# Kernel optimization log

Hardware: AMD Instinct MI355X
Metric: run time of the kernel (lower is better)

The kernel has to match this reference:

```python
import jax, jax.numpy as jnp
import numpy as np

SEQ, DM, NH, DH = 8192, 1024, 16, 64


def setup_inputs() -> dict:
    key = jax.random.key(0)
    k = jax.random.split(key, 8)
    return {
        "xs": jax.random.normal(k[0], (SEQ, DM), dtype=jnp.float32),
        "wq": jax.random.normal(k[1], (NH, DH, DM), dtype=jnp.float32),
        "wk": jax.random.normal(k[2], (NH, DH, DM), dtype=jnp.float32),
        "wv": jax.random.normal(k[3], (NH, DH, DM), dtype=jnp.float32),
        # MLP: Linear(NH*DH -> DM), gelu, Linear(DM -> NH*DH); eqx stores W as (out, in)
        "w1": jax.random.normal(k[4], (DM, NH * DH), dtype=jnp.float32) * 0.02,
        "b1": jnp.zeros((DM,), dtype=jnp.float32),
        "w2": jax.random.normal(k[5], (NH * DH, DM), dtype=jnp.float32) * 0.02,
        "b2": jnp.zeros((NH * DH,), dtype=jnp.float32),
    }


def _act(x):
    return jax.nn.elu(x) + 1.0


def reference(xs, wq, wk, wv, w1, b1, w2, b2):
    # project: (n_heads d_head d_model),(seq d_model) -> (seq n_heads d_head)
    q = jnp.einsum('hdm,sm->shd', wq, xs)
    k = jnp.einsum('hdm,sm->shd', wk, xs)
    v = jnp.einsum('hdm,sm->shd', wv, xs)

    def cell(state, qkv):
        s, z = state                      # s: (h, dk, dv), z: (h, dk)
        qt, kt, vt = qkv                  # each (h, d)
        kt = _act(kt)
        s = s + jnp.einsum('hk,hv->hkv', kt, vt)
        z = z + kt
        qa = _act(qt)
        # faithful to einops 'n_heads d_head_k d_head_v, n_heads d_head_q -> n_heads d_head_v'
        sq = jnp.einsum('hkv,hq->hv', s, qa)
        zq = jnp.einsum('hk,hq->h', z, qa)
        return (s, z), sq / zq[:, None]

    init = (jnp.zeros((NH, DH, DH), xs.dtype), jnp.zeros((NH, DH), xs.dtype))
    _, out = jax.lax.scan(cell, init, (q, k, v))   # out: (seq, h, d)
    out = out.reshape(SEQ, NH * DH)
    h = jax.nn.gelu(out @ w1.T + b1)
    return h @ w2.T + b2
```

## Files before the change

### kernel.cpp

```cpp
#include <hip/hip_runtime.h>
#include <hip/hip_bf16.h>

using bf16 = __hip_bfloat16;
typedef __attribute__((ext_vector_type(8))) short shortx8;
typedef __attribute__((ext_vector_type(4))) float f32x4;

#define SEQ 8192
#define DM 1024
#define NH 16
#define CHUNK 64
#define NC (SEQ / CHUNK)
#define NT (DM / 64)

__device__ __forceinline__ void load_lds16(const bf16* g, bf16* l) {
    __builtin_amdgcn_global_load_lds(
        (const __attribute__((address_space(1))) void*)g,
        (__attribute__((address_space(3))) void*)l, 16, 0, 0);
}

__device__ __forceinline__ unsigned ldsoff(const bf16* p) {
    return (unsigned)(unsigned long long)(__attribute__((address_space(3))) const void*)p;
}

__device__ __forceinline__ shortx8 dsr128(unsigned a) {
    shortx8 r;
    asm volatile("ds_read_b128 %0, %1" : "=v"(r) : "v"(a));
    return r;
}

__device__ __forceinline__ float bf2f(short s) {
    union { unsigned u; float f; } x;
    x.u = ((unsigned)(unsigned short)s) << 16;
    return x.f;
}

__global__ __launch_bounds__(256) void convert_all(const float* __restrict__ xs,
                                                   const float* __restrict__ wk,
                                                   const float* __restrict__ wv,
                                                   const float* __restrict__ w1,
                                                   const float* __restrict__ w2,
                                                   bf16* __restrict__ xsb,
                                                   bf16* __restrict__ wall) {
    const int b = blockIdx.x;
    const float* in;
    bf16* out;
    int blk;
    if (b < 8192) {
        in = xs; out = xsb; blk = b;
    } else {
        const int seg = (b - 8192) >> 10;
        blk = (b - 8192) & 1023;
        out = wall + (size_t)seg * DM * DM;
        if (seg == 0)      in = wk;
        else if (seg == 1) in = wv;
        else if (seg == 2) in = w1;
        else               in = w2;
    }
    size_t i = ((size_t)blk * 256 + threadIdx.x) * 4;
    float4 f = *(const float4*)(in + i);
    out[i + 0] = __float2bfloat16(f.x);
    out[i + 1] = __float2bfloat16(f.y);
    out[i + 2] = __float2bfloat16(f.z);
    out[i + 3] = __float2bfloat16(f.w);
}

template <int MODE>
__global__ __launch_bounds__(512, 2) void gemm256(const bf16* __restrict__ A,
                                                  const bf16* __restrict__ B,
                                                  void* __restrict__ Cv,
                                                  const float* __restrict__ bias,
                                                  float* __restrict__ kappa,
                                                  int N) {
    __shared__ __align__(16) bf16 As[2][256][64];
    __shared__ __align__(16) bf16 Bs[2][256][64];

    const int tid = threadIdx.x;
    const int nwg = gridDim.x * gridDim.y;
    const int bid = blockIdx.x + blockIdx.y * gridDim.x;
    const int cpx = nwg >> 3;
    const int swz = (bid & 7) * cpx + (bid >> 3);
    const int ry  = swz % gridDim.y;
    const int rx  = swz / gridDim.y;
    const int bm  = ry * 256;
    const int bn  = rx * 256;

    const int wave = tid >> 6;
    const int lane = tid & 63;
    const int wr   = wave >> 2;
    const int wc   = wave & 3;
    const int quad = lane >> 4;
    const int m16  = lane & 15;
    const int r7   = m16 & 7;
    const int wr128 = wr * 128;
    const int wc64  = wc * 64;
    const int kp0 = ((quad ^ r7) * 8);
    const int kp1 = (((4 + quad) ^ r7) * 8);

    auto stageA = [&](int half, int kt) {
        #pragma unroll
        for (int it = 0; it < 2; ++it) {
            int s = it * 512 + tid;
            int row = s >> 3, pos = s & 7;
            int g = pos ^ (row & 7);
            load_lds16(A + (size_t)(bm + half * 128 + row) * DM + kt * 64 + g * 8,
                       &As[kt & 1][half * 128 + row][pos * 8]);
        }
    };
    auto stageB = [&](int half, int kt) {
        #pragma unroll
        for (int it = 0; it < 2; ++it) {
            int s = it * 512 + tid;
            int row = s >> 3, pos = s & 7;
            int g = pos ^ (row & 7);
            load_lds16(B + (size_t)(bn + half * 128 + row) * DM + kt * 64 + g * 8,
                       &Bs[kt & 1][half * 128 + row][pos * 8]);
        }
    };

    f32x4 acc[8][4];
    #pragma unroll
    for (int i = 0; i < 8; ++i)
        #pragma unroll
        for (int j = 0; j < 4; ++j)
            #pragma unroll
            for (int r = 0; r < 4; ++r) acc[i][j][r] = 0.f;

    stageA(0, 0); stageA(1, 0); stageB(0, 0); stageB(1, 0);
    stageB(0, 1); stageB(1, 1);
    asm volatile("s_waitcnt vmcnt(4)");
    __builtin_amdgcn_s_barrier();

    shortx8 af[4][2], blo[2][2], bhi[2][2];

    #pragma unroll 1
    for (int t = 0; t < NT; ++t) {
        const int sl = t & 1;
        if (t + 1 < NT) { stageA(0, t + 1); stageA(1, t + 1); }
        #pragma unroll
        for (int i = 0; i < 4; ++i) {
            af[i][0] = dsr128(ldsoff(&As[sl][wr128 + i * 16 + m16][kp0]));
            af[i][1] = dsr128(ldsoff(&As[sl][wr128 + i * 16 + m16][kp1]));
        }
        #pragma unroll
        for (int j = 0; j < 2; ++j) {
            blo[j][0] = dsr128(ldsoff(&Bs[sl][wc64 + j * 16 + m16][kp0]));
            blo[j][1] = dsr128(ldsoff(&Bs[sl][wc64 + j * 16 + m16][kp1]));
            bhi[j][0] = dsr128(ldsoff(&Bs[sl][wc64 + (j + 2) * 16 + m16][kp0]));
            bhi[j][1] = dsr128(ldsoff(&Bs[sl][wc64 + (j + 2) * 16 + m16][kp1]));
        }
        asm volatile("s_waitcnt lgkmcnt(0)");
        __builtin_amdgcn_sched_barrier(0);
        __builtin_amdgcn_s_setprio(1);
        #pragma unroll
        for (int i = 0; i < 4; ++i)
            #pragma unroll
            for (int j = 0; j < 2; ++j) {
                acc[i][j] = __builtin_amdgcn_mfma_f32_16x16x32_bf16(af[i][0], blo[j][0], acc[i][j], 0, 0, 0);
                acc[i][j] = __builtin_amdgcn_mfma_f32_16x16x32_bf16(af[i][1], blo[j][1], acc[i][j], 0, 0, 0);
                acc[i][j + 2] = __builtin_amdgcn_mfma_f32_16x16x32_bf16(af[i][0], bhi[j][0], acc[i][j + 2], 0, 0, 0);
                acc[i][j + 2] = __builtin_amdgcn_mfma_f32_16x16x32_bf16(af[i][1], bhi[j][1], acc[i][j + 2], 0, 0, 0);
            }
        __builtin_amdgcn_s_setprio(0);
        __builtin_amdgcn_s_barrier();

        if (t + 2 < NT) { stageB(0, t + 2); stageB(1, t + 2); }
        #pragma unroll
        for (int i = 0; i < 4; ++i) {
            af[i][0] = dsr128(ldsoff(&As[sl][wr128 + 64 + i * 16 + m16][kp0]));
            af[i][1] = dsr128(ldsoff(&As[sl][wr128 + 64 + i * 16 + m16][kp1]));
        }
        asm volatile("s_waitcnt lgkmcnt(0)");
        __builtin_amdgcn_sched_barrier(0);
        __builtin_amdgcn_s_setprio(1);
        #pragma unroll
        for (int i = 0; i < 4; ++i)
            #pragma unroll
            for (int j = 0; j < 2; ++j) {
                acc[4 + i][j] = __builtin_amdgcn_mfma_f32_16x16x32_bf16(af[i][0], blo[j][0], acc[4 + i][j], 0, 0, 0);
                acc[4 + i][j] = __builtin_amdgcn_mfma_f32_16x16x32_bf16(af[i][1], blo[j][1], acc[4 + i][j], 0, 0, 0);
                acc[4 + i][j + 2] = __builtin_amdgcn_mfma_f32_16x16x32_bf16(af[i][0], bhi[j][0], acc[4 + i][j + 2], 0, 0, 0);
                acc[4 + i][j + 2] = __builtin_amdgcn_mfma_f32_16x16x32_bf16(af[i][1], bhi[j][1], acc[4 + i][j + 2], 0, 0, 0);
            }
        __builtin_amdgcn_s_setprio(0);
        if (t + 2 < NT) {
            asm volatile("s_waitcnt vmcnt(4)");
        } else {
            asm volatile("s_waitcnt vmcnt(0)");
        }
        __builtin_amdgcn_s_barrier();
    }

    if (MODE == 0) {
        const int gcol0 = bn + wc64;
        if (gcol0 < DM) {
            const int h = gcol0 >> 6;
            #pragma unroll
            for (int i = 0; i < 8; ++i) {
                #pragma unroll
                for (int r = 0; r < 4; ++r) {
                    float s = 0.f;
                    #pragma unroll
                    for (int j = 0; j < 4; ++j) {
                        float v = acc[i][j][r];
                        s += v > 0.f ? v + 1.f : __expf(v);
                    }
                    s += __shfl_xor(s, 1);
                    s += __shfl_xor(s, 2);
                    s += __shfl_xor(s, 4);
                    s += __shfl_xor(s, 8);
                    if (m16 == 0)
                        kappa[(size_t)h * SEQ + bm + wr128 + i * 16 + quad * 4 + r] = s;
                }
            }
        } else {
            bf16* vb = (bf16*)Cv;
            #pragma unroll
            for (int i = 0; i < 8; ++i) {
                int row0 = bm + wr128 + i * 16 + quad * 4;
                #pragma unroll
                for (int j = 0; j < 4; ++j) {
                    int col = gcol0 - DM + j * 16 + m16;
                    #pragma unroll
                    for (int r = 0; r < 4; ++r)
                        vb[(size_t)(row0 + r) * DM + col] = __float2bfloat16(acc[i][j][r]);
                }
            }
        }
        return;
    }

    #pragma unroll
    for (int i = 0; i < 8; ++i) {
        int row0 = bm + wr128 + i * 16 + quad * 4;
        #pragma unroll
        for (int j = 0; j < 4; ++j) {
            int col = bn + wc64 + j * 16 + m16;
            float bv = bias[col];
            #pragma unroll
            for (int r = 0; r < 4; ++r) {
                float v = acc[i][j][r] + bv;
                if (MODE == 2) {
                    float tt = tanhf(0.7978845608028654f * (v + 0.044715f * v * v * v));
                    ((bf16*)Cv)[(size_t)(row0 + r) * N + col] = __float2bfloat16(0.5f * v * (1.f + tt));
                } else {
                    ((float*)Cv)[(size_t)(row0 + r) * N + col] = v;
                }
            }
        }
    }
}

__global__ __launch_bounds__(256) void chunk_sums(const bf16* __restrict__ vb,
                                                  const float* __restrict__ kappa,
                                                  float* __restrict__ numbuf,
                                                  float* __restrict__ denbuf) {
    const int h = blockIdx.x;
    const int c = blockIdx.y * 4 + (threadIdx.x >> 6);
    const int v = threadIdx.x & 63;
    const size_t bidx = (size_t)h * NC + c;

    float kreg = kappa[(size_t)h * SEQ + c * 64 + v];
    float num = 0.f;
    const short* vrow = (const short*)vb + (size_t)(c * 64) * DM + h * 64 + v;
    #pragma unroll 8
    for (int t = 0; t < 64; ++t) {
        float kt = __shfl(kreg, t);
        num += kt * bf2f(vrow[0]);
        vrow += DM;
    }
    numbuf[bidx * 64 + v] = num;
    float d = kreg;
    #pragma unroll
    for (int off = 32; off > 0; off >>= 1) d += __shfl_xor(d, off);
    if (v == 0) denbuf[bidx] = d;
}

__global__ __launch_bounds__(256) void chunk_scan(const bf16* __restrict__ vb,
                                                  const float* __restrict__ kappa,
                                                  const float* __restrict__ numbuf,
                                                  const float* __restrict__ denbuf,
                                                  bf16* __restrict__ out) {
    const int h = blockIdx.x;
    const int c = blockIdx.y * 4 + (threadIdx.x >> 6);
    const int v = threadIdx.x & 63;
    const size_t bidx = (size_t)h * NC + c;

    float kreg = kappa[(size_t)h * SEQ + c * 64 + v];
    float num = numbuf[bidx * 64 + v];
    float den = denbuf[bidx];
    const short* vrow = (const short*)vb + (size_t)(c * 64) * DM + h * 64 + v;
    short* orow = (short*)out + (size_t)(c * 64) * DM + h * 64 + v;
    #pragma unroll 8
    for (int t = 0; t < 64; ++t) {
        float kt = __shfl(kreg, t);
        num += kt * bf2f(vrow[0]);
        den += kt;
        bf16 ob = __float2bfloat16(num / den);
        orow[0] = *(const short*)&ob;
        vrow += DM;
        orow += DM;
    }
}

__global__ __launch_bounds__(256) void prefix_state(float* __restrict__ numbuf,
                                                    float* __restrict__ denbuf) {
    const int h = blockIdx.x;
    const int wave = threadIdx.x >> 6;
    const int d = threadIdx.x & 63;
    __shared__ float tot[4][64];
    __shared__ float dtot[4];

    float val[32], dval[32];
    const int c0 = wave * 32;
    #pragma unroll
    for (int i = 0; i < 32; ++i) {
        size_t idx = (size_t)h * NC + c0 + i;
        val[i]  = numbuf[idx * 64 + d];
        dval[i] = denbuf[idx];
    }
    float run = 0.f, drun = 0.f;
    #pragma unroll
    for (int i = 0; i < 32; ++i) {
        float t = val[i];  val[i]  = run;  run  += t;
        float dt = dval[i]; dval[i] = drun; drun += dt;
    }
    tot[wave][d] = run;
    if (d == 0) dtot[wave] = drun;
    __syncthreads();
    float off = 0.f, doff = 0.f;
    for (int w = 0; w < wave; ++w) { off += tot[w][d]; doff += dtot[w]; }
    #pragma unroll
    for (int i = 0; i < 32; ++i) {
        size_t idx = (size_t)h * NC + c0 + i;
        numbuf[idx * 64 + d] = val[i] + off;
        if (d == 0) denbuf[idx] = dval[i] + doff;
    }
}

extern "C" void kernel_launch(void* const* d_in, const int* in_sizes, int n_in,
                              void* d_out, int out_size, void* d_ws, size_t ws_size,
                              hipStream_t stream) {
    const float* xs = (const float*)d_in[0];
    const float* wk = (const float*)d_in[2];
    const float* wv = (const float*)d_in[3];
    const float* w1 = (const float*)d_in[4];
    const float* b1 = (const float*)d_in[5];
    const float* w2 = (const float*)d_in[6];
    const float* b2 = (const float*)d_in[7];
    float* y = (float*)d_out;

    char* base = (char*)d_ws;
    size_t off = 0;
    auto alloc = [&](size_t b) -> char* {
        char* p = base + off;
        off += (b + 255) & ~(size_t)255;
        return p;
    };

    const size_t NMAT = (size_t)SEQ * DM;
    const size_t NW   = (size_t)DM * DM;
    bf16*  xsb    = (bf16*)alloc(NMAT * 2);
    bf16*  wall   = (bf16*)alloc(4 * NW * 2);
    bf16*  w1b    = wall + 2 * NW;
    bf16*  w2b    = wall + 3 * NW;
    bf16*  vb     = (bf16*)alloc(NMAT * 2);
    float* kappa  = (float*)alloc((size_t)NH * SEQ * 4);
    float* numbuf = (float*)alloc((size_t)NH * NC * 64 * 4);
    float* denbuf = (float*)alloc((size_t)NH * NC * 4);
    bf16*  outb   = (bf16*)alloc(NMAT * 2);
    bf16*  hb     = (bf16*)alloc(NMAT * 2);

    convert_all<<<8192 + 4 * 1024, 256, 0, stream>>>(xs, wk, wv, w1, w2,
                                                     xsb, wall);

    gemm256<0><<<dim3(2048 / 256, SEQ / 256), 512, 0, stream>>>(
        xsb, wall, vb, nullptr, kappa, 2048);

    chunk_sums<<<dim3(NH, NC / 4), 256, 0, stream>>>(vb, kappa, numbuf, denbuf);
    prefix_state<<<NH, 256, 0, stream>>>(numbuf, denbuf);
    chunk_scan<<<dim3(NH, NC / 4), 256, 0, stream>>>(vb, kappa, numbuf, denbuf,
                                                     outb);

    gemm256<2><<<dim3(DM / 256, SEQ / 256), 512, 0, stream>>>(
        outb, w1b, hb, b1, nullptr, DM);
    gemm256<3><<<dim3(DM / 256, SEQ / 256), 512, 0, stream>>>(
        hb, w2b, y, b2, nullptr, DM);
}
```

Baseline: 233.7 us.

## Use smaller-tile 128x128 GEMM kernel for MLP layers to fill all CUs

```diff
diff --git a/kernel.cpp b/kernel.cpp
--- a/kernel.cpp
+++ b/kernel.cpp
@@ -64,11 +64,9 @@
     out[i + 3] = __float2bfloat16(f.w);
 }
 
-template <int MODE>
 __global__ __launch_bounds__(512, 2) void gemm256(const bf16* __restrict__ A,
                                                   const bf16* __restrict__ B,
                                                   void* __restrict__ Cv,
-                                                  const float* __restrict__ bias,
                                                   float* __restrict__ kappa,
                                                   int N) {
     __shared__ __align__(16) bf16 As[2][256][64];
@@ -190,51 +188,110 @@
         __builtin_amdgcn_s_barrier();
     }
 
-    if (MODE == 0) {
-        const int gcol0 = bn + wc64;
-        if (gcol0 < DM) {
-            const int h = gcol0 >> 6;
-            #pragma unroll
-            for (int i = 0; i < 8; ++i) {
-                #pragma unroll
-                for (int r = 0; r < 4; ++r) {
-                    float s = 0.f;
-                    #pragma unroll
-                    for (int j = 0; j < 4; ++j) {
-                        float v = acc[i][j][r];
-                        s += v > 0.f ? v + 1.f : __expf(v);
-                    }
-                    s += __shfl_xor(s, 1);
-                    s += __shfl_xor(s, 2);
-                    s += __shfl_xor(s, 4);
-                    s += __shfl_xor(s, 8);
-                    if (m16 == 0)
-                        kappa[(size_t)h * SEQ + bm + wr128 + i * 16 + quad * 4 + r] = s;
-                }
-            }
-        } else {
-            bf16* vb = (bf16*)Cv;
-            #pragma unroll
-            for (int i = 0; i < 8; ++i) {
-                int row0 = bm + wr128 + i * 16 + quad * 4;
+    const int gcol0 = bn + wc64;
+    if (gcol0 < DM) {
+        const int h = gcol0 >> 6;
+        #pragma unroll
+        for (int i = 0; i < 8; ++i) {
+            #pragma unroll
+            for (int r = 0; r < 4; ++r) {
+                float s = 0.f;
                 #pragma unroll
                 for (int j = 0; j < 4; ++j) {
-                    int col = gcol0 - DM + j * 16 + m16;
-                    #pragma unroll
-                    for (int r = 0; r < 4; ++r)
-                        vb[(size_t)(row0 + r) * DM + col] = __float2bfloat16(acc[i][j][r]);
+                    float v = acc[i][j][r];
+                    s += v > 0.f ? v + 1.f : __expf(v);
                 }
+                s += __shfl_xor(s, 1);
+                s += __shfl_xor(s, 2);
+                s += __shfl_xor(s, 4);
+                s += __shfl_xor(s, 8);
+                if (m16 == 0)
+                    kappa[(size_t)h * SEQ + bm + wr128 + i * 16 + quad * 4 + r] = s;
             }
         }
-        return;
-    }
-
-    #pragma unroll
-    for (int i = 0; i < 8; ++i) {
-        int row0 = bm + wr128 + i * 16 + quad * 4;
+    } else {
+        bf16* vb = (bf16*)Cv;
+        #pragma unroll
+        for (int i = 0; i < 8; ++i) {
+            int row0 = bm + wr128 + i * 16 + quad * 4;
+            #pragma unroll
+            for (int j = 0; j < 4; ++j) {
+                int col = gcol0 - DM + j * 16 + m16;
+                #pragma unroll
+                for (int r = 0; r < 4; ++r)
+                    vb[(size_t)(row0 + r) * DM + col] = __float2bfloat16(acc[i][j][r]);
+            }
+        }
+    }
+}
+
+template <int MODE>
+__global__ __launch_bounds__(256) void gemm_nt(const bf16* __restrict__ A,
+                                               const bf16* __restrict__ B,
+                                               void* __restrict__ Cv,
+                                               const float* __restrict__ bias,
+                                               int N) {
+    __shared__ bf16 As[128][64];
+    __shared__ bf16 Bs[128][64];
+
+    const int tid  = threadIdx.x;
+    const int L    = blockIdx.x + blockIdx.y * gridDim.x;
+    const int ry   = L % gridDim.y;
+    const int rx   = L / gridDim.y;
+    const int bm   = ry * 128;
+    const int bn   = rx * 128;
+    const int wave = tid >> 6;
+    const int lane = tid & 63;
+    const int wm   = (wave >> 1) * 64;
+    const int wn   = (wave & 1) * 64;
+    const int quad = lane >> 4;
+    const int m16  = lane & 15;
+    const int r7   = m16 & 7;
+
+    f32x4 acc[4][4];
+    #pragma unroll
+    for (int i = 0; i < 4; ++i)
+        #pragma unroll
+        for (int j = 0; j < 4; ++j)
+            #pragma unroll
+            for (int r = 0; r < 4; ++r) acc[i][j][r] = 0.f;
+
+    for (int k0 = 0; k0 < DM; k0 += 64) {
+        #pragma unroll
+        for (int it = 0; it < 4; ++it) {
+            int s = it * 256 + tid;
+            int row = s >> 3, pos = s & 7;
+            int g = pos ^ (row & 7);
+            load_lds16(A + (size_t)(bm + row) * DM + k0 + g * 8, &As[row][pos * 8]);
+            load_lds16(B + (size_t)(bn + row) * DM + k0 + g * 8, &Bs[row][pos * 8]);
+        }
+        __syncthreads();
+
+        #pragma unroll
+        for (int kx = 0; kx < 2; ++kx) {
+            const int p = ((kx << 2) + quad) ^ r7;
+            shortx8 af[4], bfr[4];
+            #pragma unroll
+            for (int i = 0; i < 4; ++i)
+                af[i] = *(const shortx8*)&As[wm + i * 16 + m16][p * 8];
+            #pragma unroll
+            for (int j = 0; j < 4; ++j)
+                bfr[j] = *(const shortx8*)&Bs[wn + j * 16 + m16][p * 8];
+            #pragma unroll
+            for (int i = 0; i < 4; ++i)
+                #pragma unroll
+                for (int j = 0; j < 4; ++j)
+                    acc[i][j] = __builtin_amdgcn_mfma_f32_16x16x32_bf16(af[i], bfr[j], acc[i][j], 0, 0, 0);
+        }
+        __syncthreads();
+    }
+
+    #pragma unroll
+    for (int i = 0; i < 4; ++i) {
+        int row0 = bm + wm + i * 16 + quad * 4;
         #pragma unroll
         for (int j = 0; j < 4; ++j) {
-            int col = bn + wc64 + j * 16 + m16;
+            int col = bn + wn + j * 16 + m16;
             float bv = bias[col];
             #pragma unroll
             for (int r = 0; r < 4; ++r) {
@@ -373,16 +430,16 @@
     convert_all<<<8192 + 4 * 1024, 256, 0, stream>>>(xs, wk, wv, w1, w2,
                                                      xsb, wall);
 
-    gemm256<0><<<dim3(2048 / 256, SEQ / 256), 512, 0, stream>>>(
-        xsb, wall, vb, nullptr, kappa, 2048);
+    gemm256<<<dim3(2048 / 256, SEQ / 256), 512, 0, stream>>>(
+        xsb, wall, vb, kappa, 2048);
 
     chunk_sums<<<dim3(NH, NC / 4), 256, 0, stream>>>(vb, kappa, numbuf, denbuf);
     prefix_state<<<NH, 256, 0, stream>>>(numbuf, denbuf);
     chunk_scan<<<dim3(NH, NC / 4), 256, 0, stream>>>(vb, kappa, numbuf, denbuf,
                                                      outb);
 
-    gemm256<2><<<dim3(DM / 256, SEQ / 256), 512, 0, stream>>>(
-        outb, w1b, hb, b1, nullptr, DM);
-    gemm256<3><<<dim3(DM / 256, SEQ / 256), 512, 0, stream>>>(
-        hb, w2b, y, b2, nullptr, DM);
-}
+    gemm_nt<2><<<dim3(DM / 128, SEQ / 128), 256, 0, stream>>>(
+        outb, w1b, hb, b1, DM);
+    gemm_nt<3><<<dim3(DM / 128, SEQ / 128), 256, 0, stream>>>(
+        hb, w2b, y, b2, DM);
+}
```

Result: faster. 212.1 us (-9.2%).
